# Kernel tuning notes

Measured on AMD Instinct MI355X. Metric: run time of the kernel, lower is better.

## Reference

```python
import jax, jax.numpy as jnp
import numpy as np

B, C, H, W, K = 2, 64, 192, 192, 7
PAD = K // 2
EPS = 1e-6


def _win_idx(L):
    # NATTEN border handling: window is shifted (not zero-padded) to stay in-bounds.
    i = jnp.arange(L)
    start = jnp.clip(i - PAD, 0, L - K)            # [L] window start per query pos
    win = start[:, None] + jnp.arange(K)[None]     # [L,K] absolute key positions
    pb = (K - 1) - (i - start)                     # [L] rpb start index per query pos
    pbi = pb[:, None] + jnp.arange(K)[None]        # [L,K] rpb table indices
    return win, pbi


def setup_inputs() -> dict:
    key = jax.random.key(0)
    ks = jax.random.split(key, 10)
    g = jax.random.normal(ks[0], (B, C, H, W), jnp.float32)
    cd = jax.random.uniform(ks[1], (B, 1, H, W), dtype=jnp.float32)
    dense = jax.random.uniform(ks[2], (B, 1, H, W), dtype=jnp.float32)
    sel = jax.random.uniform(ks[3], (B, 1, H, W)) < 0.05
    sd = jnp.where(sel, dense, 0.0)
    mask = (jax.random.uniform(ks[4], (B, 1, H, W)) < 0.5).astype(jnp.float32)
    ln_w = 1.0 + 0.02 * jax.random.normal(ks[5], (C,), jnp.float32)
    ln_b = 0.02 * jax.random.normal(ks[6], (C,), jnp.float32)
    conv_w = 0.05 * jax.random.normal(ks[7], (2 * C, C + 1), jnp.float32)  # 1x1 conv
    conv_b = 0.02 * jax.random.normal(ks[8], (2 * C,), jnp.float32)
    rpb = 0.02 * jax.random.normal(ks[9], (1, 2 * K - 1, 2 * K - 1), jnp.float32)
    return {"g": g, "cd": cd, "sd": sd, "mask": mask,
            "ln_w": ln_w, "ln_b": ln_b, "conv_w": conv_w, "conv_b": conv_b, "rpb": rpb}


def reference(g, cd, sd, mask, ln_w, ln_b, conv_w, conv_b, rpb):
    # LayerNorm2d: normalize over channel dim per spatial location
    mu = g.mean(axis=1, keepdims=True)
    var = ((g - mu) ** 2).mean(axis=1, keepdims=True)
    gn = (g - mu) * jax.lax.rsqrt(var + EPS)
    gn = gn * ln_w[None, :, None, None] + ln_b[None, :, None, None]

    z = jnp.concatenate([gn, cd], axis=1)                      # [B,C+1,H,W]
    qk = jnp.einsum('bchw,oc->bohw', z, conv_w) + conv_b[None, :, None, None]
    q, k = qk[:, :C], qk[:, C:]
    k = k * mask

    qc = q.transpose(0, 2, 3, 1)                               # [B,H,W,C] single head
    kc = k.transpose(0, 2, 3, 1)
    rwin, rpbi = _win_idx(H)
    cwin, cpbi = _win_idx(W)

    # NATTEN qk + relative position bias over 7x7 neighborhoods
    k_win = kc[:, rwin][:, :, :, cwin]                         # [B,H,K,W,K,C]
    attn = jnp.einsum('bhwc,bhiwjc->bhwij', qc, k_win)         # [B,H,W,K,K]
    bias = rpb[0][rpbi][:, :, cpbi]                            # [H,K,W,K]
    attn = attn + bias.transpose(0, 2, 1, 3)[None]
    a = jax.nn.softmax(attn.reshape(B, H, W, K * K), axis=-1).reshape(B, H, W, K, K)

    # NATTEN av with v = cd (head_dim 1)
    v_win = cd[:, 0][:, rwin][:, :, :, cwin]                   # [B,H,K,W,K]
    cd_out = jnp.einsum('bhwij,bhiwj->bhw', a, v_win)[:, None]  # [B,1,H,W]
    m_win = mask[:, 0][:, rwin][:, :, :, cwin]
    mask_out = jnp.einsum('bhwij,bhiwj->bhw', a, m_win)[:, None]

    # NYU / SDR post-processing
    cd_out = cd_out * mask + cd * (1.0 - mask)
    valid = sd > 0
    cd_out = jnp.where(valid, sd, cd_out)
    mask_out = jnp.where(valid, mask, mask_out)
    return cd_out, mask_out
```

## Files before the change

### kernel.cpp

```cpp
#include <hip/hip_runtime.h>

constexpr int NB = 2;
constexpr int NC = 64;
constexpr int NH = 192;
constexpr int NW = 192;
constexpr int NK = 7;
constexpr int NHW = NH * NW;
constexpr int NPIX = NB * NHW;
constexpr float EPS = 1e-6f;

__global__ __launch_bounds__(256) void qk_gemm(
    const float* __restrict__ g, const float* __restrict__ cd,
    const float* __restrict__ mask,
    const float* __restrict__ ln_w, const float* __restrict__ ln_b,
    const float* __restrict__ conv_w, const float* __restrict__ conv_b,
    float* __restrict__ qbuf, float* __restrict__ kbuf)
{
    __shared__ float Z[65][128];
    __shared__ float WTc[33][128];

    int tid = threadIdx.x;
    int p0 = blockIdx.x * 128;
    int b  = p0 / NHW;
    int hw0 = p0 - b * NHW;

    int px = tid >> 1;
    int hf = tid & 1;
    const float* gp = g + (size_t)(b * NC + hf * 32) * NHW + (hw0 + px);
    float vals[32];
    float s = 0.f, sq = 0.f;
#pragma unroll
    for (int j = 0; j < 32; ++j) {
        float v = gp[(size_t)j * NHW];
        vals[j] = v; s += v; sq += v * v;
    }
    s  += __shfl_xor(s, 1);
    sq += __shfl_xor(sq, 1);
    float mu   = s * (1.f / 64.f);
    float rstd = rsqrtf(sq * (1.f / 64.f) - mu * mu + EPS);
#pragma unroll
    for (int j = 0; j < 32; ++j) {
        int c = hf * 32 + j;
        Z[c][px] = (vals[j] - mu) * rstd * ln_w[c] + ln_b[c];
    }
    if (hf) Z[64][px] = cd[p0 + px];

    int og = tid >> 4;
    int pg = tid & 15;
    float acc[8][8];
#pragma unroll
    for (int oi = 0; oi < 8; ++oi)
#pragma unroll
        for (int pj = 0; pj < 8; ++pj) acc[oi][pj] = 0.f;

    for (int cc = 0; cc < 65; cc += 33) {
        int nr = (65 - cc < 33) ? (65 - cc) : 33;
        __syncthreads();
        if (tid < 128) {
            int o = tid;
            for (int r = 0; r < nr; ++r)
                WTc[r][o] = conv_w[o * 65 + cc + r];
        }
        __syncthreads();
        for (int r = 0; r < nr; ++r) {
            float4 w0 = *(const float4*)&WTc[r][8 * og];
            float4 w1 = *(const float4*)&WTc[r][8 * og + 4];
            float4 z0 = *(const float4*)&Z[cc + r][8 * pg];
            float4 z1 = *(const float4*)&Z[cc + r][8 * pg + 4];
            float w8[8] = {w0.x, w0.y, w0.z, w0.w, w1.x, w1.y, w1.z, w1.w};
            float z8[8] = {z0.x, z0.y, z0.z, z0.w, z1.x, z1.y, z1.z, z1.w};
#pragma unroll
            for (int oi = 0; oi < 8; ++oi)
#pragma unroll
                for (int pj = 0; pj < 8; ++pj)
                    acc[oi][pj] = fmaf(w8[oi], z8[pj], acc[oi][pj]);
        }
    }

    int o0  = og * 8;
    int pxb = pg * 8;
    float4 ba = *(const float4*)&conv_b[o0];
    float4 bb = *(const float4*)&conv_b[o0 + 4];
    float bia[8] = {ba.x, ba.y, ba.z, ba.w, bb.x, bb.y, bb.z, bb.w};
    bool isq = (o0 < 64);
    float m8[8];
    if (!isq) {
        float4 ma = *(const float4*)&mask[p0 + pxb];
        float4 mc = *(const float4*)&mask[p0 + pxb + 4];
        m8[0]=ma.x; m8[1]=ma.y; m8[2]=ma.z; m8[3]=ma.w;
        m8[4]=mc.x; m8[5]=mc.y; m8[6]=mc.z; m8[7]=mc.w;
    }
    float* base = isq ? (qbuf + (size_t)(b * NC + o0) * NHW + hw0 + pxb)
                      : (kbuf + (size_t)(b * NC + o0 - 64) * NHW + hw0 + pxb);
#pragma unroll
    for (int oi = 0; oi < 8; ++oi) {
        float v[8];
#pragma unroll
        for (int pj = 0; pj < 8; ++pj) {
            float t = acc[oi][pj] + bia[oi];
            v[pj] = isq ? t : t * m8[pj];
        }
        float* dst = base + (size_t)oi * NHW;
        *(float4*)&dst[0] = make_float4(v[0], v[1], v[2], v[3]);
        *(float4*)&dst[4] = make_float4(v[4], v[5], v[6], v[7]);
    }
}

struct TrueC  { static constexpr bool value = true;  };
struct FalseC { static constexpr bool value = false; };

__global__ __launch_bounds__(256) void attn_tile(
    const float* __restrict__ qbuf, const float* __restrict__ kbuf,
    const float* __restrict__ cd, const float* __restrict__ sd,
    const float* __restrict__ mask, const float* __restrict__ rpb,
    float* __restrict__ out_cd, float* __restrict__ out_mask)
{
    __shared__ float kst[4][2][350];
    __shared__ float xch[49][2][64];
    __shared__ float cdt[350];
    __shared__ float mt [350];
    __shared__ float rpbt[169];

    int tid  = threadIdx.x;
    int g    = tid >> 6;
    int lane = tid & 63;
    int tx   = lane & 7;
    int ty   = lane >> 3;

    int bid = blockIdx.x;
    int swz = (bid & 7) * 72 + (bid >> 3);
    int bw = swz % 12;
    int t2 = swz / 12;
    int bh = t2 % 24;
    int b  = t2 / 24;
    int w0 = bw * 16, h0 = bh * 8;

    int h   = h0 + ty;
    int wpx = w0 + 2 * tx;
    int rs  = min(max(h - 3, 0), NH - NK);
    int cs0 = min(max(wpx - 3, 0), NW - NK);
    int cs1 = min(max(wpx - 2, 0), NW - NK);
    int d1  = cs1 - cs0;
    int ktb = (rs - (h0 - 3)) * 25 + (cs0 - (w0 - 3));

    const float* cdb = cd   + (size_t)b * NHW;
    const float* msb = mask + (size_t)b * NHW;
    for (int e = tid; e < 308; e += 256) {
        int r = e / 22, c = e - r * 22;
        int gr = min(max(h0 - 3 + r, 0), NH - 1);
        int gc = min(max(w0 - 3 + c, 0), NW - 1);
        cdt[r * 25 + c] = cdb[gr * NW + gc];
        mt [r * 25 + c] = msb[gr * NW + gc];
    }
    if (tid < 169) rpbt[tid] = rpb[tid];

    int soff[5], slds[5];
#pragma unroll
    for (int s = 0; s < 5; ++s) {
        int e = lane + 64 * s;
        int r = e / 22, c = e - r * 22;
        int gr = min(max(h0 - 3 + r, 0), NH - 1);
        int gc = min(max(w0 - 3 + c, 0), NW - 1);
        bool act = e < 308;
        soff[s] = act ? (gr * NW + gc) : 0;
        slds[s] = act ? (r * 25 + c) : 348;
    }

    const float* kb = kbuf + (size_t)(b * NC + g * 16) * NHW;
    const float* qb = qbuf + (size_t)(b * NC + g * 16) * NHW + h * NW + wpx;

    float at0[49], at1[49];
#pragma unroll
    for (int n = 0; n < 49; ++n) { at0[n] = 0.f; at1[n] = 0.f; }

    float* k0 = &kst[g][0][0];
    float* k1 = &kst[g][1][0];

    auto run = [&](auto edgec) {
        constexpr bool EDGE = decltype(edgec)::value;
        float st[5];
#pragma unroll
        for (int s = 0; s < 5; ++s) st[s] = kb[soff[s]];
#pragma unroll
        for (int s = 0; s < 5; ++s) k0[slds[s]] = st[s];
        float2 qA = *(const float2*)qb;
        float2 qB = *(const float2*)(qb + NHW);
        for (int i = 0; i < 16; ++i) {
            if (i + 1 < 16) {
                const float* kb2 = kb + (size_t)(i + 1) * NHW;
#pragma unroll
                for (int s = 0; s < 5; ++s) st[s] = kb2[soff[s]];
            }
            float2 q = qA; qA = qB;
            if (i + 2 < 16) qB = *(const float2*)(qb + (size_t)(i + 2) * NHW);
            const float* kt = ((i & 1) ? k1 : k0) + ktb;
#pragma unroll
            for (int r = 0; r < 7; ++r) {
                const float* kr = kt + r * 25;
                float v[8];
#pragma unroll
                for (int j = 0; j < 8; ++j) v[j] = kr[j];
#pragma unroll
                for (int j = 0; j < 7; ++j)
                    at0[r * 7 + j] = fmaf(q.x, v[j], at0[r * 7 + j]);
#pragma unroll
                for (int j = 0; j < 7; ++j) {
                    float u;
                    if constexpr (EDGE) u = d1 ? v[j + 1] : v[j];
                    else                u = v[j + 1];
                    at1[r * 7 + j] = fmaf(q.y, u, at1[r * 7 + j]);
                }
            }
            if (i + 1 < 16) {
                float* nk = (i & 1) ? k0 : k1;
#pragma unroll
                for (int s = 0; s < 5; ++s) nk[slds[s]] = st[s];
            }
        }
    };
    if (bw == 0 || bw == 11) run(TrueC{}); else run(FalseC{});

    __syncthreads();
    if (g == 3) {
#pragma unroll
        for (int n = 0; n < 49; ++n) {
            xch[n][0][lane] = at0[n]; xch[n][1][lane] = at1[n];
        }
    }
    __syncthreads();
    if (g == 2) {
#pragma unroll
        for (int n = 0; n < 49; ++n) {
            xch[n][0][lane] += at0[n]; xch[n][1][lane] += at1[n];
        }
    }
    __syncthreads();
    if (g == 0) {
#pragma unroll
        for (int n = 0; n < 49; ++n) {
            xch[n][0][lane] += at0[n]; xch[n][1][lane] += at1[n];
        }
    }
    __syncthreads();
    int pr  = 6 - (h - rs);
    int pc0 = 6 - (wpx - cs0);
    int pc1 = 6 - (wpx + 1 - cs1);
    if (g == 1) {
#pragma unroll
        for (int n = 0; n < 49; ++n) {
            at0[n] += xch[n][0][lane]; at1[n] += xch[n][1][lane];
        }
#pragma unroll
        for (int r = 0; r < 7; ++r)
#pragma unroll
            for (int j = 0; j < 7; ++j) {
                at0[r * 7 + j] += rpbt[(pr + r) * 13 + pc0 + j];
                at1[r * 7 + j] += rpbt[(pr + r) * 13 + pc1 + j];
            }
#pragma unroll
        for (int n = 0; n < 49; ++n) {
            xch[n][0][lane] = at0[n]; xch[n][1][lane] = at1[n];
        }
    }
    __syncthreads();
    if (g == 0) {
#pragma unroll
        for (int n = 0; n < 49; ++n) {
            at0[n] = xch[n][0][lane]; at1[n] = xch[n][1][lane];
        }
    }
    if (g >= 2) return;

    float mx0 = -1e30f, mx1 = -1e30f;
#pragma unroll
    for (int n = 0; n < 49; ++n) {
        mx0 = fmaxf(mx0, at0[n]); mx1 = fmaxf(mx1, at1[n]);
    }
    float sm0 = 0.f, sm1 = 0.f;
#pragma unroll
    for (int n = 0; n < 49; ++n) {
        at0[n] = __expf(at0[n] - mx0); sm0 += at0[n];
        at1[n] = __expf(at1[n] - mx1); sm1 += at1[n];
    }

    const float* vt = (g ? mt : cdt) + ktb;
    float sv0 = 0.f, sv1 = 0.f;
#pragma unroll
    for (int r = 0; r < 7; ++r) {
        const float* vr = vt + r * 25;
        float v[8];
#pragma unroll
        for (int j = 0; j < 8; ++j) v[j] = vr[j];
#pragma unroll
        for (int j = 0; j < 7; ++j) {
            sv0 = fmaf(at0[r * 7 + j], v[j], sv0);
            float u = d1 ? v[j + 1] : v[j];
            sv1 = fmaf(at1[r * 7 + j], u, sv1);
        }
    }
    sv0 /= sm0; sv1 /= sm1;

    int p = b * NHW + h * NW + wpx;
    float2 sdv = *(const float2*)(sd + p);
    int ci = (ty + 3) * 25 + (2 * tx + 3);
    float mc0 = mt[ci], mc1 = mt[ci + 1];
    if (g == 0) {
        float cdc0 = cdt[ci], cdc1 = cdt[ci + 1];
        float co0 = sv0 * mc0 + cdc0 * (1.f - mc0);
        float co1 = sv1 * mc1 + cdc1 * (1.f - mc1);
        if (sdv.x > 0.f) co0 = sdv.x;
        if (sdv.y > 0.f) co1 = sdv.y;
        *(float2*)(out_cd + p) = make_float2(co0, co1);
    } else {
        float o0 = (sdv.x > 0.f) ? mc0 : sv0;
        float o1 = (sdv.y > 0.f) ? mc1 : sv1;
        *(float2*)(out_mask + p) = make_float2(o0, o1);
    }
}

extern "C" void kernel_launch(void* const* d_in, const int* in_sizes, int n_in,
                              void* d_out, int out_size, void* d_ws, size_t ws_size,
                              hipStream_t stream) {
    const float* g      = (const float*)d_in[0];
    const float* cd     = (const float*)d_in[1];
    const float* sd     = (const float*)d_in[2];
    const float* mask   = (const float*)d_in[3];
    const float* ln_w   = (const float*)d_in[4];
    const float* ln_b   = (const float*)d_in[5];
    const float* conv_w = (const float*)d_in[6];
    const float* conv_b = (const float*)d_in[7];
    const float* rpb    = (const float*)d_in[8];

    float* out  = (float*)d_out;
    float* qbuf = (float*)d_ws;
    float* kbuf = qbuf + (size_t)NB * NC * NHW;

    qk_gemm<<<dim3(NPIX / 128), dim3(256), 0, stream>>>(
        g, cd, mask, ln_w, ln_b, conv_w, conv_b, qbuf, kbuf);
    attn_tile<<<dim3(NB * 24 * 12), dim3(256), 0, stream>>>(
        qbuf, kbuf, cd, sd, mask, rpb, out, out + NPIX);
}
```

Before: 135.5 us.

## Split cross-group attention reduction by pixel and assign softmax per pixel

The four K-split groups' partial 7x7 logits are now reduced through shared memory in three phases, with each phase handling the two pixels in different groups. This replaces a four-barrier serial chain and a broadcast step. Afterwards group 0 handles pixel 0 and group 1 handles pixel 1, each adding the position bias, running the softmax, and computing both the cd and mask weighted sums itself. The aim is fewer barriers and less serial LDS traffic, at the cost of doing both value reductions per thread and writing scalar outputs instead of float2.

```diff
diff --git a/kernel.cpp b/kernel.cpp
--- a/kernel.cpp
+++ b/kernel.cpp
@@ -220,102 +220,92 @@
     };
     if (bw == 0 || bw == 11) run(TrueC{}); else run(FalseC{});
 
+    if (g == 1) {
+#pragma unroll
+        for (int n = 0; n < 49; ++n) xch[n][0][lane] = at0[n];
+    } else if (g == 0) {
+#pragma unroll
+        for (int n = 0; n < 49; ++n) xch[n][1][lane] = at1[n];
+    }
+    __syncthreads();
+    if (g == 2) {
+#pragma unroll
+        for (int n = 0; n < 49; ++n) xch[n][0][lane] += at0[n];
+    } else if (g == 3) {
+#pragma unroll
+        for (int n = 0; n < 49; ++n) xch[n][1][lane] += at1[n];
+    }
     __syncthreads();
     if (g == 3) {
 #pragma unroll
-        for (int n = 0; n < 49; ++n) {
-            xch[n][0][lane] = at0[n]; xch[n][1][lane] = at1[n];
-        }
+        for (int n = 0; n < 49; ++n) xch[n][0][lane] += at0[n];
+    } else if (g == 2) {
+#pragma unroll
+        for (int n = 0; n < 49; ++n) xch[n][1][lane] += at1[n];
     }
     __syncthreads();
-    if (g == 2) {
-#pragma unroll
-        for (int n = 0; n < 49; ++n) {
-            xch[n][0][lane] += at0[n]; xch[n][1][lane] += at1[n];
-        }
-    }
-    __syncthreads();
-    if (g == 0) {
-#pragma unroll
-        for (int n = 0; n < 49; ++n) {
-            xch[n][0][lane] += at0[n]; xch[n][1][lane] += at1[n];
-        }
-    }
-    __syncthreads();
+    if (g >= 2) return;
+
     int pr  = 6 - (h - rs);
     int pc0 = 6 - (wpx - cs0);
     int pc1 = 6 - (wpx + 1 - cs1);
-    if (g == 1) {
-#pragma unroll
-        for (int n = 0; n < 49; ++n) {
-            at0[n] += xch[n][0][lane]; at1[n] += xch[n][1][lane];
-        }
-#pragma unroll
-        for (int r = 0; r < 7; ++r)
-#pragma unroll
-            for (int j = 0; j < 7; ++j) {
-                at0[r * 7 + j] += rpbt[(pr + r) * 13 + pc0 + j];
-                at1[r * 7 + j] += rpbt[(pr + r) * 13 + pc1 + j];
-            }
-#pragma unroll
-        for (int n = 0; n < 49; ++n) {
-            xch[n][0][lane] = at0[n]; xch[n][1][lane] = at1[n];
-        }
-    }
-    __syncthreads();
+    int pcx = (g == 0) ? pc0 : pc1;
+    int dd  = (g == 0) ? 0 : d1;
+
+    float aF[49];
     if (g == 0) {
 #pragma unroll
-        for (int n = 0; n < 49; ++n) {
-            at0[n] = xch[n][0][lane]; at1[n] = xch[n][1][lane];
-        }
-    }
-    if (g >= 2) return;
-
-    float mx0 = -1e30f, mx1 = -1e30f;
+        for (int n = 0; n < 49; ++n) aF[n] = at0[n] + xch[n][0][lane];
+    } else {
+#pragma unroll
+        for (int n = 0; n < 49; ++n) aF[n] = at1[n] + xch[n][1][lane];
+    }
+#pragma unroll
+    for (int r = 0; r < 7; ++r)
+#pragma unroll
+        for (int j = 0; j < 7; ++j)
+            aF[r * 7 + j] += rpbt[(pr + r) * 13 + pcx + j];
+
+    float mx = -1e30f;
+#pragma unroll
+    for (int n = 0; n < 49; ++n) mx = fmaxf(mx, aF[n]);
+    float sm = 0.f;
 #pragma unroll
     for (int n = 0; n < 49; ++n) {
-        mx0 = fmaxf(mx0, at0[n]); mx1 = fmaxf(mx1, at1[n]);
-    }
-    float sm0 = 0.f, sm1 = 0.f;
-#pragma unroll
-    for (int n = 0; n < 49; ++n) {
-        at0[n] = __expf(at0[n] - mx0); sm0 += at0[n];
-        at1[n] = __expf(at1[n] - mx1); sm1 += at1[n];
-    }
-
-    const float* vt = (g ? mt : cdt) + ktb;
-    float sv0 = 0.f, sv1 = 0.f;
+        aF[n] = __expf(aF[n] - mx);
+        sm += aF[n];
+    }
+
+    const float* vtc = cdt + ktb;
+    const float* vtm = mt  + ktb;
+    float sc = 0.f, sv = 0.f;
 #pragma unroll
     for (int r = 0; r < 7; ++r) {
-        const float* vr = vt + r * 25;
-        float v[8];
-#pragma unroll
-        for (int j = 0; j < 8; ++j) v[j] = vr[j];
+        const float* vr = vtc + r * 25;
+        const float* wr = vtm + r * 25;
+        float v[8], w[8];
+#pragma unroll
+        for (int j = 0; j < 8; ++j) { v[j] = vr[j]; w[j] = wr[j]; }
 #pragma unroll
         for (int j = 0; j < 7; ++j) {
-            sv0 = fmaf(at0[r * 7 + j], v[j], sv0);
-            float u = d1 ? v[j + 1] : v[j];
-            sv1 = fmaf(at1[r * 7 + j], u, sv1);
-        }
-    }
-    sv0 /= sm0; sv1 /= sm1;
-
-    int p = b * NHW + h * NW + wpx;
-    float2 sdv = *(const float2*)(sd + p);
-    int ci = (ty + 3) * 25 + (2 * tx + 3);
-    float mc0 = mt[ci], mc1 = mt[ci + 1];
-    if (g == 0) {
-        float cdc0 = cdt[ci], cdc1 = cdt[ci + 1];
-        float co0 = sv0 * mc0 + cdc0 * (1.f - mc0);
-        float co1 = sv1 * mc1 + cdc1 * (1.f - mc1);
-        if (sdv.x > 0.f) co0 = sdv.x;
-        if (sdv.y > 0.f) co1 = sdv.y;
-        *(float2*)(out_cd + p) = make_float2(co0, co1);
-    } else {
-        float o0 = (sdv.x > 0.f) ? mc0 : sv0;
-        float o1 = (sdv.y > 0.f) ? mc1 : sv1;
-        *(float2*)(out_mask + p) = make_float2(o0, o1);
-    }
+            float a  = aF[r * 7 + j];
+            float uC = dd ? v[j + 1] : v[j];
+            float uM = dd ? w[j + 1] : w[j];
+            sc = fmaf(a, uC, sc);
+            sv = fmaf(a, uM, sv);
+        }
+    }
+    sc /= sm; sv /= sm;
+
+    int p = b * NHW + h * NW + wpx + g;
+    float sdc = sd[p];
+    int ci = (ty + 3) * 25 + (2 * tx + 3) + g;
+    float mc  = mt[ci];
+    float cdc = cdt[ci];
+    float co = sc * mc + cdc * (1.f - mc);
+    if (sdc > 0.f) co = sdc;
+    out_cd[p]   = co;
+    out_mask[p] = (sdc > 0.f) ? mc : sv;
 }
 
 extern "C" void kernel_launch(void* const* d_in, const int* in_sizes, int n_in,
```

Result: faster. 132.4 us (-2.3%).
